# Kernel optimization log

Measured on AMD Instinct MI355X. Metric: run time of the kernel, lower is better.

## Reference

```python
import jax, jax.numpy as jnp
import numpy as np
from jax import lax

B, C, H, W = 2, 128, 192, 192
HEADS, WS, SS = 4, 8, 4
HID = 256  # int(C * expansion=2.0)
EPS = 1e-6


def _rpe_index(ws):
    coords = np.stack(np.meshgrid(np.arange(ws), np.arange(ws), indexing='ij')).reshape(2, -1)
    rel = (coords[:, :, None] - coords[:, None, :]).transpose(1, 2, 0)
    rel[:, :, 0] += ws - 1
    rel[:, :, 1] += ws - 1
    rel[:, :, 0] *= 2 * ws - 1
    return rel.sum(-1)  # (ws^2, ws^2) int index into rpe_table

RPE_IDX = _rpe_index(WS)


def _attn_mask(hp, wp, ws, ss):
    # Swin-style shifted-window mask, built once for static (hp, wp).
    img = np.zeros((hp, wp))
    cnt = 0
    for hs in (slice(0, -ws), slice(-ws, -ss), slice(-ss, None)):
        for wsl in (slice(0, -ws), slice(-ws, -ss), slice(-ss, None)):
            img[hs, wsl] = cnt
            cnt += 1
    mw = img.reshape(hp // ws, ws, wp // ws, ws).transpose(0, 2, 1, 3).reshape(-1, ws * ws)
    am = mw[:, None, :] - mw[:, :, None]
    return np.where(am != 0, -np.inf, 0.0).astype(np.float32)

MASK = jnp.asarray(_attn_mask(H, W, WS, SS))  # (nW, T, T)


def rmsnorm(x, s, b):
    # RMSNorm2d: variance over channel dim, computed in fp32.
    var = jnp.mean(jnp.square(x.astype(jnp.float32)), axis=1, keepdims=True)
    rms = jnp.sqrt(var + EPS).astype(x.dtype)
    return s[None, :, None, None] * x / rms + b[None, :, None, None]


def conv1x1(x, w, b):
    return jnp.einsum('oc,bchw->bohw', w, x) + b[None, :, None, None]


def dwconv3x3(x, w, b):
    y = lax.conv_general_dilated(x, w, (1, 1), 'SAME', feature_group_count=w.shape[0],
                                 dimension_numbers=('NCHW', 'OIHW', 'NCHW'))
    return y + b[None, :, None, None]


def gelu(x):
    return jax.nn.gelu(x, approximate=False)  # matches torch nn.GELU default (erf)


def conv_gated_block(x, s, b, w1, b1, wd, bd, w2, b2, beta):
    y = rmsnorm(x, s, b)
    y = conv1x1(y, w1, b1)
    y = dwconv3x3(y, wd, bd)
    u, v = jnp.split(y, 2, axis=1)
    y = conv1x1(u * gelu(v), w2, b2)
    return x + beta * y


def gated_ffn(x, s, b, w1, b1, w2, b2, gamma):
    y = rmsnorm(x, s, b)
    y = conv1x1(y, w1, b1)
    u, v = jnp.split(y, 2, axis=1)
    y = conv1x1(u * gelu(v), w2, b2)
    return x + gamma * y


def window_attention(x, qkv_w, qkv_b, rpe_table, proj_w, proj_b):
    b, c, h, w = x.shape
    hd = c // HEADS
    ws, ws2 = WS, WS * WS
    # H, W chosen divisible by ws, so _pad_to_window is a no-op here.
    x = jnp.roll(x, (-SS, -SS), axis=(2, 3))
    qkv = jnp.einsum('oc,bchw->bhwo', qkv_w, x) + qkv_b  # (B,H,W,3C)
    qkv = qkv.reshape(b, h // ws, ws, w // ws, ws, 3 * c).transpose(0, 1, 3, 2, 4, 5)
    qkv = qkv.reshape(-1, ws2, 3, HEADS, hd).transpose(2, 0, 3, 1, 4)  # (3, B*nW, nh, T, hd)
    q, k, v = qkv[0], qkv[1], qkv[2]
    attn = jnp.einsum('wnqd,wnkd->wnqk', q, k) * (hd ** -0.5)
    rpe = rpe_table[RPE_IDX.reshape(-1)].reshape(ws2, ws2, HEADS).transpose(2, 0, 1)  # (nh,T,T)
    nW = (h // ws) * (w // ws)
    attn = attn.reshape(b, nW, HEADS, ws2, ws2) + rpe[None, None] + MASK[None, :, None]
    attn = jax.nn.softmax(attn, axis=-1).reshape(-1, HEADS, ws2, ws2)
    out = jnp.einsum('wnqk,wnkd->wnqd', attn, v)
    out = out.transpose(0, 2, 1, 3).reshape(-1, ws2, c)
    out = out @ proj_w.T + proj_b  # nn.Linear
    out = out.reshape(b, h // ws, w // ws, ws, ws, c).transpose(0, 1, 3, 2, 4, 5).reshape(b, h, w, c)
    out = jnp.roll(out, (SS, SS), axis=(1, 2))
    return out.transpose(0, 3, 1, 2)


def setup_inputs():
    key = jax.random.key(0)
    ks = jax.random.split(key, 10)
    f = jnp.float32

    def nrm(k, shape, std=0.02):
        return jax.random.normal(k, shape, dtype=f) * std

    return {
        'x': jax.random.normal(ks[0], (B, C, H, W), dtype=f),
        'cg_s': jnp.ones((C,), f), 'cg_b': jnp.zeros((C,), f),
        'pw1_w': nrm(ks[1], (2 * HID, C)), 'pw1_b': jnp.zeros((2 * HID,), f),
        'dw_w': nrm(ks[2], (2 * HID, 1, 3, 3)), 'dw_b': jnp.zeros((2 * HID,), f),
        'pw2_w': nrm(ks[3], (C, HID)), 'pw2_b': jnp.zeros((C,), f),
        'beta': jnp.float32(0.5),
        'at_s': jnp.ones((C,), f), 'at_b': jnp.zeros((C,), f),
        'qkv_w': nrm(ks[4], (3 * C, C)), 'qkv_b': jnp.zeros((3 * C,), f),
        'rpe_table': nrm(ks[5], ((2 * WS - 1) ** 2, HEADS)),
        'proj_w': nrm(ks[6], (C, C)), 'proj_b': jnp.zeros((C,), f),
        'alpha': jnp.float32(0.5),
        'ff_s': jnp.ones((C,), f), 'ff_b': jnp.zeros((C,), f),
        'fc1_w': nrm(ks[7], (2 * HID, C)), 'fc1_b': jnp.zeros((2 * HID,), f),
        'fc2_w': nrm(ks[8], (C, HID)), 'fc2_b': jnp.zeros((C,), f),
        'gamma': jnp.float32(0.5),
    }


def reference(x, cg_s, cg_b, pw1_w, pw1_b, dw_w, dw_b, pw2_w, pw2_b, beta,
              at_s, at_b, qkv_w, qkv_b, rpe_table, proj_w, proj_b, alpha,
              ff_s, ff_b, fc1_w, fc1_b, fc2_w, fc2_b, gamma):
    x = conv_gated_block(x, cg_s, cg_b, pw1_w, pw1_b, dw_w, dw_b, pw2_w, pw2_b, beta)
    x = x + alpha * window_attention(rmsnorm(x, at_s, at_b), qkv_w, qkv_b, rpe_table, proj_w, proj_b)
    x = gated_ffn(x, ff_s, ff_b, fc1_w, fc1_b, fc2_w, fc2_b, gamma)
    return x
```

## Files before the change

### kernel.cpp

```cpp
#include <hip/hip_runtime.h>
#include <hip/hip_bf16.h>
#include <math.h>

#define HW   36864
#define BHW  73728

typedef float f32x4 __attribute__((ext_vector_type(4)));
typedef short short8 __attribute__((ext_vector_type(8)));

__device__ __forceinline__ unsigned f2bf(float f) {
    unsigned u = __float_as_uint(f);
    return (u + 0x7fffu + ((u >> 16) & 1u)) >> 16;
}
__device__ __forceinline__ float bf2f(unsigned short s) {
    return __uint_as_float(((unsigned)s) << 16);
}
__device__ __forceinline__ float gelu_erf(float v) {
    return v * 0.5f * (1.0f + erff(v * 0.70710678118654752f));
}

__global__ __launch_bounds__(256)
void wconv_kernel(const float* __restrict__ w1, const float* __restrict__ w2,
                  const float* __restrict__ wq, const float* __restrict__ wp,
                  const float* __restrict__ wf1, const float* __restrict__ wf2,
                  const float* __restrict__ dww, const float* __restrict__ fb1,
                  ushort* __restrict__ o1, ushort* __restrict__ o2, ushort* __restrict__ oq,
                  ushort* __restrict__ op, ushort* __restrict__ of1, ushort* __restrict__ of2,
                  float* __restrict__ dwt, float* __restrict__ bg)
{
    int i = blockIdx.x * 256 + threadIdx.x;
    if      (i <  65536) o1 [i         ] = (ushort)f2bf(w1 [i         ]);
    else if (i <  98304) o2 [i -  65536] = (ushort)f2bf(w2 [i -  65536]);
    else if (i < 147456) oq [i -  98304] = (ushort)f2bf(wq [i -  98304]);
    else if (i < 163840) op [i - 147456] = (ushort)f2bf(wp [i - 147456]);
    else if (i < 229376) {
        int j = i - 163840;
        int col = j >> 7, k = j & 127;
        of1[j] = (ushort)f2bf(wf1[((size_t)((col & 1) * 256 + (col >> 1))) * 128 + k]);
    }
    else if (i < 262144) of2[i - 229376] = (ushort)f2bf(wf2[i - 229376]);
    else if (i < 266752) {
        int j = i - 262144;
        int tap = j >> 9, c = j & 511;
        dwt[j] = dww[c * 9 + tap];
    }
    else if (i < 267264) {
        int j = i - 266752;
        bg[j] = fb1[(j & 1) * 256 + (j >> 1)];
    }
}

__global__ __launch_bounds__(256)
void rmsnorm_t_kernel(const float* __restrict__ src, const float* __restrict__ s,
                      const float* __restrict__ bi, __hip_bfloat16* __restrict__ dst)
{
    int P = blockIdx.x * 256 + threadIdx.x;
    int b = P / HW, pp = P - b * HW;
    const float* xb = src + (size_t)b * 128 * HW + pp;
    float ss = 0.f;
#pragma unroll 8
    for (int c = 0; c < 128; ++c) { float v = xb[(size_t)c * HW]; ss = fmaf(v, v, ss); }
    float inv = 1.0f / sqrtf(ss * 0.0078125f + 1e-6f);
    unsigned* drow = (unsigned*)(dst + (size_t)P * 128);
#pragma unroll 4
    for (int c = 0; c < 128; c += 2) {
        float v0 = fmaf(s[c]     * xb[(size_t)c * HW],       inv, bi[c]);
        float v1 = fmaf(s[c + 1] * xb[(size_t)(c + 1) * HW], inv, bi[c + 1]);
        drow[c >> 1] = f2bf(v0) | (f2bf(v1) << 16);
    }
}

template<int K, int MODE>
__global__ __launch_bounds__(256)
void gemm_kernel(const __hip_bfloat16* __restrict__ Abf, const __hip_bfloat16* __restrict__ Wbf,
                 const float* __restrict__ bias, int N,
                 __hip_bfloat16* __restrict__ outb,
                 const float* __restrict__ rsrc, float* __restrict__ rdst,
                 const float* __restrict__ scale,
                 const float* __restrict__ rms_s, const float* __restrict__ rms_b,
                 __hip_bfloat16* __restrict__ xn)
{
    constexpr int SMEM = (MODE == 3) ? 56320 : ((MODE == 1) ? 34816 : 16384);
    __shared__ char smem[SMEM];
    short* sA = (short*)smem;
    short* sB = sA + 4096;
    float* sEp = (float*)smem;
    float* sPar = (float*)(smem + 34816);
    float* sInv = (float*)(smem + 39168);
    ushort* sXn = (ushort*)(smem + 39424);

    const short* A = (const short*)Abf;
    const short* W = (const short*)Wbf;

    int t = threadIdx.x;
    int lane = t & 63, wv = t >> 6;
    int wm = wv & 1, wn = wv >> 1;
    int m0 = blockIdx.x * 128;
    int n0 = blockIdx.y * 128;
    int q = lane >> 4, r16 = lane & 15;

    f32x4 acc[4][4];
#pragma unroll
    for (int nt = 0; nt < 4; ++nt) {
        float bv = bias[n0 + wn * 64 + nt * 16 + r16];
#pragma unroll
        for (int mt = 0; mt < 4; ++mt) acc[mt][nt] = (f32x4){bv, bv, bv, bv};
    }

    for (int kk = 0; kk < K; kk += 32) {
#pragma unroll
        for (int i = 0; i < 2; ++i) {
            int rbase = wv * 32 + i * 16;
            int row = rbase + (lane >> 2);
            int kc = (lane & 3) ^ ((row >> 1) & 3);
            const short* ga = A + (size_t)(m0 + row) * K + kk + kc * 8;
            const short* gb = W + (size_t)(n0 + row) * K + kk + kc * 8;
            __builtin_amdgcn_global_load_lds((const __attribute__((address_space(1))) void*)ga,
                                             (__attribute__((address_space(3))) void*)(sA + rbase * 32), 16, 0, 0);
            __builtin_amdgcn_global_load_lds((const __attribute__((address_space(1))) void*)gb,
                                             (__attribute__((address_space(3))) void*)(sB + rbase * 32), 16, 0, 0);
        }
        __syncthreads();

        short8 af[4], bf[4];
#pragma unroll
        for (int mt = 0; mt < 4; ++mt) {
            int r = wm * 64 + mt * 16 + r16;
            af[mt] = *(const short8*)(sA + (r * 4 + (q ^ ((r >> 1) & 3))) * 8);
        }
#pragma unroll
        for (int nt = 0; nt < 4; ++nt) {
            int r = wn * 64 + nt * 16 + r16;
            bf[nt] = *(const short8*)(sB + (r * 4 + (q ^ ((r >> 1) & 3))) * 8);
        }
#pragma unroll
        for (int mt = 0; mt < 4; ++mt)
#pragma unroll
            for (int nt = 0; nt < 4; ++nt)
                acc[mt][nt] = __builtin_amdgcn_mfma_f32_16x16x32_bf16(af[mt], bf[nt], acc[mt][nt], 0, 0, 0);
        __syncthreads();
    }

    if constexpr (MODE == 0) {
        ushort* ob = (ushort*)outb;
#pragma unroll
        for (int mt = 0; mt < 4; ++mt) {
            int row0 = m0 + wm * 64 + mt * 16 + q * 4;
#pragma unroll
            for (int nt = 0; nt < 4; ++nt) {
                int col = n0 + wn * 64 + nt * 16 + r16;
#pragma unroll
                for (int rg = 0; rg < 4; ++rg)
                    ob[(size_t)(row0 + rg) * N + col] = (ushort)f2bf(acc[mt][nt][rg]);
            }
        }
    } else if constexpr (MODE == 2) {
        ushort* ob = (ushort*)outb;
        int parity = r16 & 1;
#pragma unroll
        for (int mt = 0; mt < 4; ++mt) {
            int row0 = m0 + wm * 64 + mt * 16 + q * 4;
#pragma unroll
            for (int nt = 0; nt < 4; ++nt) {
                int ch = (n0 + wn * 64 + nt * 16 + r16) >> 1;
#pragma unroll
                for (int rg = 0; rg < 4; ++rg) {
                    float val = acc[mt][nt][rg];
                    float part = __shfl_xor(val, 1);
                    float uu = parity ? part : val;
                    float vv = parity ? val : part;
                    float g = uu * gelu_erf(vv);
                    if (!parity)
                        ob[(size_t)(row0 + rg) * 256 + ch] = (ushort)f2bf(g);
                }
            }
        }
    } else {
        float sc = scale[0];
        for (int h = 0; h < 2; ++h) {
            __syncthreads();
            if (wm == h) {
#pragma unroll
                for (int mt = 0; mt < 4; ++mt)
#pragma unroll
                    for (int nt = 0; nt < 4; ++nt) {
                        int c = wn * 64 + nt * 16 + r16;
                        int px = mt * 16 + q * 4;
#pragma unroll
                        for (int rg = 0; rg < 4; ++rg)
                            sEp[c * 68 + px + rg] = acc[mt][nt][rg];
                    }
            }
            __syncthreads();
            int c16 = t >> 4, l16 = t & 15;
            int p0 = m0 + h * 64 + l16 * 4;
            int b = p0 / HW, pp = p0 - b * HW;
            f32x4 ov[8];
            f32x4 ps = (f32x4){0.f, 0.f, 0.f, 0.f};
#pragma unroll
            for (int i = 0; i < 8; ++i) {
                int c = c16 + i * 16;
                f32x4 v = *(const f32x4*)&sEp[c * 68 + l16 * 4];
                size_t gi = (size_t)(b * 128 + c) * HW + pp;
                f32x4 r = *(const f32x4*)&rsrc[gi];
                f32x4 o = r + sc * v;
                *(f32x4*)&rdst[gi] = o;
                if constexpr (MODE == 3) {
                    ov[i] = o;
#pragma unroll
                    for (int rg = 0; rg < 4; ++rg) ps[rg] = fmaf(o[rg], o[rg], ps[rg]);
                }
            }
            if constexpr (MODE == 3) {
#pragma unroll
                for (int rg = 0; rg < 4; ++rg) sPar[(l16 * 4 + rg) * 17 + c16] = ps[rg];
                __syncthreads();
                if (t < 64) {
                    float ssum = 0.f;
#pragma unroll
                    for (int j = 0; j < 16; ++j) ssum += sPar[t * 17 + j];
                    sInv[t] = 1.0f / sqrtf(ssum * 0.0078125f + 1e-6f);
                }
                __syncthreads();
                float iv[4];
#pragma unroll
                for (int rg = 0; rg < 4; ++rg) iv[rg] = sInv[l16 * 4 + rg];
#pragma unroll
                for (int i = 0; i < 8; ++i) {
                    int c = c16 + i * 16;
                    float scs = rms_s[c], bcs = rms_b[c];
#pragma unroll
                    for (int rg = 0; rg < 4; ++rg)
                        sXn[(l16 * 4 + rg) * 132 + c] = (ushort)f2bf(fmaf(scs * ov[i][rg], iv[rg], bcs));
                }
                __syncthreads();
                {
                    int px = t >> 2, qd = t & 3;
                    const ushort* src = sXn + px * 132 + qd * 32;
                    ushort* dst = (ushort*)xn + (size_t)(m0 + h * 64 + px) * 128 + qd * 32;
#pragma unroll
                    for (int g = 0; g < 4; ++g)
                        *(short8*)(dst + g * 8) = *(const short8*)(src + g * 8);
                }
            }
        }
    }
}

__global__ __launch_bounds__(256)
void dwgate_kernel(const __hip_bfloat16* __restrict__ t1, const float* __restrict__ dwt,
                   const float* __restrict__ dwb, __hip_bfloat16* __restrict__ tg)
{
    int t = threadIdx.x;
    int c8 = t & 31, pxl = t >> 5;
    int bx = blockIdx.x;
    int wseg = bx % 24; int tmp = bx / 24;
    int hp2 = tmp % 96; int b = tmp / 96;
    int h0 = hp2 * 2, w = wseg * 8 + pxl;
    int cu = c8 * 8;
    const ushort* t1u = (const ushort*)t1;

    float au[2][8], av[2][8];
    {
        f32x4 b0 = *(const f32x4*)(dwb + cu);
        f32x4 b1 = *(const f32x4*)(dwb + cu + 4);
        f32x4 b2 = *(const f32x4*)(dwb + 256 + cu);
        f32x4 b3 = *(const f32x4*)(dwb + 256 + cu + 4);
#pragma unroll
        for (int e = 0; e < 4; ++e) {
            au[0][e] = au[1][e] = b0[e]; au[0][e + 4] = au[1][e + 4] = b1[e];
            av[0][e] = av[1][e] = b2[e]; av[0][e + 4] = av[1][e + 4] = b3[e];
        }
    }
#pragma unroll
    for (int r = 0; r < 4; ++r) {
        int hh = h0 - 1 + r;
        if (hh < 0 || hh >= 192) continue;
#pragma unroll
        for (int dxi = 0; dxi < 3; ++dxi) {
            int w2 = w + dxi - 1;
            if (w2 < 0 || w2 >= 192) continue;
            const ushort* urow = t1u + (size_t)(b * HW + hh * 192 + w2) * 512 + cu;
            short8 u8 = *(const short8*)urow;
            short8 v8 = *(const short8*)(urow + 256);
#pragma unroll
            for (int py = 0; py < 2; ++py) {
                int dy = r - 1 - py;
                if (dy < -1 || dy > 1) continue;
                int tap = (dy + 1) * 3 + dxi;
                f32x4 wu0 = *(const f32x4*)(dwt + tap * 512 + cu);
                f32x4 wu1 = *(const f32x4*)(dwt + tap * 512 + cu + 4);
                f32x4 wv0 = *(const f32x4*)(dwt + tap * 512 + 256 + cu);
                f32x4 wv1 = *(const f32x4*)(dwt + tap * 512 + 256 + cu + 4);
#pragma unroll
                for (int e = 0; e < 4; ++e) {
                    au[py][e]     = fmaf(wu0[e], bf2f((ushort)u8[e]),     au[py][e]);
                    au[py][e + 4] = fmaf(wu1[e], bf2f((ushort)u8[e + 4]), au[py][e + 4]);
                    av[py][e]     = fmaf(wv0[e], bf2f((ushort)v8[e]),     av[py][e]);
                    av[py][e + 4] = fmaf(wv1[e], bf2f((ushort)v8[e + 4]), av[py][e + 4]);
                }
            }
        }
    }
#pragma unroll
    for (int py = 0; py < 2; ++py) {
        short8 o8;
#pragma unroll
        for (int e = 0; e < 8; ++e) o8[e] = (short)(ushort)f2bf(au[py][e] * gelu_erf(av[py][e]));
        int gp = b * HW + (h0 + py) * 192 + w;
        *(short8*)((ushort*)tg + (size_t)gp * 256 + cu) = o8;
    }
}

__device__ __forceinline__ int wpix(int wh, int ww, int m) {
    int ty = m >> 3, tx = m & 7;
    int hs = wh * 8 + ty + 4; if (hs >= 192) hs -= 192;
    int wsc = ww * 8 + tx + 4; if (wsc >= 192) wsc -= 192;
    return hs * 192 + wsc;
}
__device__ __forceinline__ int wreg(int wh, int ww, int m) {
    int hr = wh * 8 + (m >> 3), wr = ww * 8 + (m & 7);
    return ((hr < 184) ? 0 : (hr < 188) ? 1 : 2) * 3 +
           ((wr < 184) ? 0 : (wr < 188) ? 1 : 2);
}

__global__ __launch_bounds__(256)
void attn_kernel(const __hip_bfloat16* __restrict__ qkv, const float* __restrict__ rpe,
                 __hip_bfloat16* __restrict__ attnout)
{
    __shared__ char smem[54288];
    int t = threadIdx.x;
    int lane = t & 63, head = t >> 6;
    int wh = blockIdx.x / 24, ww = blockIdx.x % 24;
    int b = blockIdx.y;
    int q = lane >> 4, r16 = lane & 15;

    float* rpe_s = (float*)(smem + 50688);
    for (int i = t; i < 900; i += 256) rpe_s[i] = rpe[i];

    char* Pbuf  = smem + head * 12672;
    char* VTbuf = Pbuf + 8448;
    const ushort* qkvu = (const ushort*)qkv;

    short8 aq[4], bk[4];
#pragma unroll
    for (int mt = 0; mt < 4; ++mt) {
        int pix = wpix(wh, ww, mt * 16 + r16);
        const ushort* rowp = qkvu + (size_t)(b * HW + pix) * 384 + head * 32 + q * 8;
        aq[mt] = *(const short8*)rowp;
        bk[mt] = *(const short8*)(rowp + 128);
    }
    {
        int pix = wpix(wh, ww, lane);
        const ushort* vp = qkvu + (size_t)(b * HW + pix) * 384 + 256 + head * 32;
        ushort* vt = (ushort*)VTbuf;
#pragma unroll
        for (int g = 0; g < 4; ++g) {
            short8 v8 = *(const short8*)(vp + g * 8);
#pragma unroll
            for (int e = 0; e < 8; ++e) vt[(g * 8 + e) * 66 + lane] = (ushort)v8[e];
        }
    }
    __syncthreads();

    f32x4 s[4][4];
#pragma unroll
    for (int mt = 0; mt < 4; ++mt)
#pragma unroll
        for (int nt = 0; nt < 4; ++nt) s[mt][nt] = (f32x4){0.f, 0.f, 0.f, 0.f};
#pragma unroll
    for (int mt = 0; mt < 4; ++mt)
#pragma unroll
        for (int nt = 0; nt < 4; ++nt)
            s[mt][nt] = __builtin_amdgcn_mfma_f32_16x16x32_bf16(aq[mt], bk[nt], s[mt][nt], 0, 0, 0);

    bool edge = (wh == 23) || (ww == 23);
    int tyj[4], txj[4], rgj[4];
#pragma unroll
    for (int nt = 0; nt < 4; ++nt) {
        int j = nt * 16 + r16;
        tyj[nt] = j >> 3; txj[nt] = j & 7;
        rgj[nt] = wreg(wh, ww, j);
    }
    float rinv[4][4];
#pragma unroll
    for (int mt = 0; mt < 4; ++mt) {
#pragma unroll
        for (int rg = 0; rg < 4; ++rg) {
            int i = mt * 16 + q * 4 + rg;
            int tyi = i >> 3, txi = i & 7;
            int rgi = edge ? wreg(wh, ww, i) : 0;
            float mx = -INFINITY;
#pragma unroll
            for (int nt = 0; nt < 4; ++nt) {
                float v = s[mt][nt][rg] * 0.17677669529663689f
                        + rpe_s[((tyi - tyj[nt] + 7) * 15 + (txi - txj[nt] + 7)) * 4 + head];
                if (edge && rgi != rgj[nt]) v = -INFINITY;
                s[mt][nt][rg] = v;
                mx = fmaxf(mx, v);
            }
            mx = fmaxf(mx, __shfl_xor(mx, 1));
            mx = fmaxf(mx, __shfl_xor(mx, 2));
            mx = fmaxf(mx, __shfl_xor(mx, 4));
            mx = fmaxf(mx, __shfl_xor(mx, 8));
            float sum = 0.f;
#pragma unroll
            for (int nt = 0; nt < 4; ++nt) {
                float e = __expf(s[mt][nt][rg] - mx);
                s[mt][nt][rg] = e;
                sum += e;
            }
            sum += __shfl_xor(sum, 1);
            sum += __shfl_xor(sum, 2);
            sum += __shfl_xor(sum, 4);
            sum += __shfl_xor(sum, 8);
            rinv[mt][rg] = 1.0f / sum;
        }
    }

    ushort* Pu = (ushort*)Pbuf;
#pragma unroll
    for (int mt = 0; mt < 4; ++mt)
#pragma unroll
        for (int rg = 0; rg < 4; ++rg) {
            int i = mt * 16 + q * 4 + rg;
#pragma unroll
            for (int nt = 0; nt < 4; ++nt)
                Pu[i * 66 + nt * 16 + r16] = (ushort)f2bf(s[mt][nt][rg]);
        }
    __syncthreads();

    f32x4 o[4][2];
#pragma unroll
    for (int mt = 0; mt < 4; ++mt) { o[mt][0] = (f32x4){0,0,0,0}; o[mt][1] = (f32x4){0,0,0,0}; }
    const uint* Pw = (const uint*)Pbuf;
    const uint* Vw = (const uint*)VTbuf;
#pragma unroll
    for (int ks = 0; ks < 2; ++ks) {
        short8 ap[4];
#pragma unroll
        for (int mt = 0; mt < 4; ++mt) {
            int base = (mt * 16 + r16) * 33 + ks * 16 + q * 4;
            uint d0 = Pw[base], d1 = Pw[base + 1], d2 = Pw[base + 2], d3 = Pw[base + 3];
            union { uint u[4]; short8 s8; } cv; cv.u[0] = d0; cv.u[1] = d1; cv.u[2] = d2; cv.u[3] = d3;
            ap[mt] = cv.s8;
        }
        short8 bv[2];
#pragma unroll
        for (int nt = 0; nt < 2; ++nt) {
            int base = (nt * 16 + r16) * 33 + ks * 16 + q * 4;
            uint d0 = Vw[base], d1 = Vw[base + 1], d2 = Vw[base + 2], d3 = Vw[base + 3];
            union { uint u[4]; short8 s8; } cv; cv.u[0] = d0; cv.u[1] = d1; cv.u[2] = d2; cv.u[3] = d3;
            bv[nt] = cv.s8;
        }
#pragma unroll
        for (int mt = 0; mt < 4; ++mt)
#pragma unroll
            for (int nt = 0; nt < 2; ++nt)
                o[mt][nt] = __builtin_amdgcn_mfma_f32_16x16x32_bf16(ap[mt], bv[nt], o[mt][nt], 0, 0, 0);
    }
    __syncthreads();

    float* Of = (float*)Pbuf;
#pragma unroll
    for (int mt = 0; mt < 4; ++mt)
#pragma unroll
        for (int rg = 0; rg < 4; ++rg) {
            int i = mt * 16 + q * 4 + rg;
            float sc = rinv[mt][rg];
            Of[i * 33 + r16]      = o[mt][0][rg] * sc;
            Of[i * 33 + 16 + r16] = o[mt][1][rg] * sc;
        }
    __syncthreads();
    {
        int pix = wpix(wh, ww, lane);
        ushort* ob = (ushort*)attnout + (size_t)(b * HW + pix) * 128 + head * 32;
#pragma unroll
        for (int g = 0; g < 4; ++g) {
            short8 o8;
#pragma unroll
            for (int e = 0; e < 8; ++e) o8[e] = (short)(ushort)f2bf(Of[lane * 33 + g * 8 + e]);
            *(short8*)(ob + g * 8) = o8;
        }
    }
}

extern "C" void kernel_launch(void* const* d_in, const int* in_sizes, int n_in,
                              void* d_out, int out_size, void* d_ws, size_t ws_size,
                              hipStream_t stream)
{
    const float* x     = (const float*)d_in[0];
    const float* cg_s  = (const float*)d_in[1];
    const float* cg_b  = (const float*)d_in[2];
    const float* pw1_w = (const float*)d_in[3];
    const float* pw1_b = (const float*)d_in[4];
    const float* dw_w  = (const float*)d_in[5];
    const float* dw_b  = (const float*)d_in[6];
    const float* pw2_w = (const float*)d_in[7];
    const float* pw2_b = (const float*)d_in[8];
    const float* beta  = (const float*)d_in[9];
    const float* at_s  = (const float*)d_in[10];
    const float* at_b  = (const float*)d_in[11];
    const float* qkv_w = (const float*)d_in[12];
    const float* qkv_b = (const float*)d_in[13];
    const float* rpe   = (const float*)d_in[14];
    const float* proj_w= (const float*)d_in[15];
    const float* proj_b= (const float*)d_in[16];
    const float* alpha = (const float*)d_in[17];
    const float* ff_s  = (const float*)d_in[18];
    const float* ff_b  = (const float*)d_in[19];
    const float* fc1_w = (const float*)d_in[20];
    const float* fc1_b = (const float*)d_in[21];
    const float* fc2_w = (const float*)d_in[22];
    const float* fc2_b = (const float*)d_in[23];
    const float* gamma = (const float*)d_in[24];
    float* out = (float*)d_out;

    char* ws = (char*)d_ws;
    __hip_bfloat16* Xn    = (__hip_bfloat16*)ws;
    __hip_bfloat16* t1    = (__hip_bfloat16*)(ws + 18874368);
    __hip_bfloat16* qkvb  = t1;
    __hip_bfloat16* tg    = (__hip_bfloat16*)(ws + 94371840);
    __hip_bfloat16* attno = tg;
    char* wsw = ws + 132120576;
    ushort* w1b  = (ushort*)(wsw);
    ushort* w2b  = (ushort*)(wsw + 131072);
    ushort* wqb  = (ushort*)(wsw + 196608);
    ushort* wpb  = (ushort*)(wsw + 294912);
    ushort* wf1b = (ushort*)(wsw + 327680);
    ushort* wf2b = (ushort*)(wsw + 458752);
    float*  dwt  = (float*) (wsw + 524288);
    float*  bg1  = (float*) (wsw + 542720);

    wconv_kernel<<<1044, 256, 0, stream>>>(pw1_w, pw2_w, qkv_w, proj_w, fc1_w, fc2_w, dw_w, fc1_b,
                                           w1b, w2b, wqb, wpb, wf1b, wf2b, dwt, bg1);

    rmsnorm_t_kernel<<<288, 256, 0, stream>>>(x, cg_s, cg_b, Xn);
    gemm_kernel<128, 0><<<dim3(576, 4), 256, 0, stream>>>(Xn, (__hip_bfloat16*)w1b, pw1_b, 512, t1,
                                                          nullptr, nullptr, nullptr, nullptr, nullptr, nullptr);
    dwgate_kernel<<<4608, 256, 0, stream>>>(t1, dwt, dw_b, tg);
    gemm_kernel<256, 3><<<dim3(576, 1), 256, 0, stream>>>(tg, (__hip_bfloat16*)w2b, pw2_b, 128, nullptr,
                                                          x, out, beta, at_s, at_b, Xn);

    gemm_kernel<128, 0><<<dim3(576, 3), 256, 0, stream>>>(Xn, (__hip_bfloat16*)wqb, qkv_b, 384, qkvb,
                                                          nullptr, nullptr, nullptr, nullptr, nullptr, nullptr);
    attn_kernel<<<dim3(576, 2), 256, 0, stream>>>(qkvb, rpe, attno);
    gemm_kernel<128, 3><<<dim3(576, 1), 256, 0, stream>>>(attno, (__hip_bfloat16*)wpb, proj_b, 128, nullptr,
                                                          out, out, alpha, ff_s, ff_b, Xn);

    gemm_kernel<128, 2><<<dim3(576, 4), 256, 0, stream>>>(Xn, (__hip_bfloat16*)wf1b, bg1, 512, tg,
                                                          nullptr, nullptr, nullptr, nullptr, nullptr, nullptr);
    gemm_kernel<256, 1><<<dim3(576, 1), 256, 0, stream>>>(tg, (__hip_bfloat16*)wf2b, fc2_b, 128, nullptr,
                                                          out, out, gamma, nullptr, nullptr, nullptr);
}
```

Baseline: 410.5 us.

## Stage GEMM epilogue stores through LDS and retile depthwise gate kernel

The MODE 0 and MODE 2 GEMM epilogues now write bf16 results into a padded shared-memory tile and then emit coalesced 16-byte row stores, replacing scattered 2-byte global writes. The depthwise-conv gate kernel is retiled so each thread handles 4 channels over 4 output rows. It preloads all 9 tap weights into registers and uses branchless clamped loads, which cuts reloads of weights and overlapping input rows. This adds extra syncs and LDS traffic in the GEMMs and raises register pressure in the dwconv kernel, with launch bounds set for 3 blocks per SIMD.

```diff
diff --git a/kernel.cpp b/kernel.cpp
--- a/kernel.cpp
+++ b/kernel.cpp
@@ -7,6 +7,7 @@
 
 typedef float f32x4 __attribute__((ext_vector_type(4)));
 typedef short short8 __attribute__((ext_vector_type(8)));
+typedef short s16x4 __attribute__((ext_vector_type(4)));
 
 __device__ __forceinline__ unsigned f2bf(float f) {
     unsigned u = __float_as_uint(f);
@@ -80,7 +81,8 @@
                  const float* __restrict__ rms_s, const float* __restrict__ rms_b,
                  __hip_bfloat16* __restrict__ xn)
 {
-    constexpr int SMEM = (MODE == 3) ? 56320 : ((MODE == 1) ? 34816 : 16384);
+    constexpr int SMEM = (MODE == 3) ? 56320 : ((MODE == 1) ? 34816 :
+                         ((MODE == 0) ? 17408 : 16384));
     __shared__ char smem[SMEM];
     short* sA = (short*)smem;
     short* sB = sA + 4096;
@@ -142,37 +144,62 @@
     }
 
     if constexpr (MODE == 0) {
+        ushort* sC = (ushort*)smem;
         ushort* ob = (ushort*)outb;
-#pragma unroll
-        for (int mt = 0; mt < 4; ++mt) {
-            int row0 = m0 + wm * 64 + mt * 16 + q * 4;
-#pragma unroll
-            for (int nt = 0; nt < 4; ++nt) {
-                int col = n0 + wn * 64 + nt * 16 + r16;
-#pragma unroll
-                for (int rg = 0; rg < 4; ++rg)
-                    ob[(size_t)(row0 + rg) * N + col] = (ushort)f2bf(acc[mt][nt][rg]);
+        for (int h = 0; h < 2; ++h) {
+            __syncthreads();
+            if (wm == h) {
+#pragma unroll
+                for (int mt = 0; mt < 4; ++mt)
+#pragma unroll
+                    for (int nt = 0; nt < 4; ++nt) {
+                        int row = mt * 16 + q * 4;
+                        int col = wn * 64 + nt * 16 + r16;
+#pragma unroll
+                        for (int rg = 0; rg < 4; ++rg)
+                            sC[(row + rg) * 136 + col] = (ushort)f2bf(acc[mt][nt][rg]);
+                    }
+            }
+            __syncthreads();
+            int px = t >> 2, ck = t & 3;
+            size_t base = (size_t)(m0 + h * 64 + px) * N + n0;
+#pragma unroll
+            for (int g = 0; g < 4; ++g) {
+                int co = (ck * 4 + g) * 8;
+                *(short8*)(ob + base + co) = *(const short8*)(sC + px * 136 + co);
             }
         }
     } else if constexpr (MODE == 2) {
+        ushort* sG = (ushort*)smem;
         ushort* ob = (ushort*)outb;
         int parity = r16 & 1;
-#pragma unroll
-        for (int mt = 0; mt < 4; ++mt) {
-            int row0 = m0 + wm * 64 + mt * 16 + q * 4;
-#pragma unroll
-            for (int nt = 0; nt < 4; ++nt) {
-                int ch = (n0 + wn * 64 + nt * 16 + r16) >> 1;
-#pragma unroll
-                for (int rg = 0; rg < 4; ++rg) {
-                    float val = acc[mt][nt][rg];
-                    float part = __shfl_xor(val, 1);
-                    float uu = parity ? part : val;
-                    float vv = parity ? val : part;
-                    float g = uu * gelu_erf(vv);
-                    if (!parity)
-                        ob[(size_t)(row0 + rg) * 256 + ch] = (ushort)f2bf(g);
-                }
+        for (int h = 0; h < 2; ++h) {
+            __syncthreads();
+            if (wm == h) {
+#pragma unroll
+                for (int mt = 0; mt < 4; ++mt)
+#pragma unroll
+                    for (int nt = 0; nt < 4; ++nt) {
+                        int row = mt * 16 + q * 4;
+                        int gch = (wn * 64 + nt * 16 + r16) >> 1;
+#pragma unroll
+                        for (int rg = 0; rg < 4; ++rg) {
+                            float val = acc[mt][nt][rg];
+                            float part = __shfl_xor(val, 1);
+                            float uu = parity ? part : val;
+                            float vv = parity ? val : part;
+                            float g = uu * gelu_erf(vv);
+                            if (!parity) sG[(row + rg) * 72 + gch] = (ushort)f2bf(g);
+                        }
+                    }
+            }
+            __syncthreads();
+            int px = t >> 2, ck = t & 3;
+            size_t base = (size_t)(m0 + h * 64 + px) * 256 + (n0 >> 1);
+#pragma unroll
+            for (int g = 0; g < 2; ++g) {
+                int co = (ck * 2 + g) * 8;
+                *(short8*)(ob + base + co) = *(const short8*)(sG + px * 72 + co);
             }
         }
     } else {
@@ -247,68 +274,73 @@
     }
 }
 
-__global__ __launch_bounds__(256)
+__global__ __launch_bounds__(256, 3)
 void dwgate_kernel(const __hip_bfloat16* __restrict__ t1, const float* __restrict__ dwt,
                    const float* __restrict__ dwb, __hip_bfloat16* __restrict__ tg)
 {
     int t = threadIdx.x;
-    int c8 = t & 31, pxl = t >> 5;
+    int tc = t & 15;
+    int tp = t >> 4;
     int bx = blockIdx.x;
-    int wseg = bx % 24; int tmp = bx / 24;
-    int hp2 = tmp % 96; int b = tmp / 96;
-    int h0 = hp2 * 2, w = wseg * 8 + pxl;
-    int cu = c8 * 8;
+    int wseg = bx % 12; int tmp = bx / 12;
+    int hq = tmp % 48; int b = tmp / 48;
+    int cu = blockIdx.y * 64 + tc * 4;
+    int h0 = hq * 4;
+    int w = wseg * 16 + tp;
     const ushort* t1u = (const ushort*)t1;
 
-    float au[2][8], av[2][8];
-    {
-        f32x4 b0 = *(const f32x4*)(dwb + cu);
-        f32x4 b1 = *(const f32x4*)(dwb + cu + 4);
-        f32x4 b2 = *(const f32x4*)(dwb + 256 + cu);
-        f32x4 b3 = *(const f32x4*)(dwb + 256 + cu + 4);
-#pragma unroll
-        for (int e = 0; e < 4; ++e) {
-            au[0][e] = au[1][e] = b0[e]; au[0][e + 4] = au[1][e + 4] = b1[e];
-            av[0][e] = av[1][e] = b2[e]; av[0][e + 4] = av[1][e + 4] = b3[e];
-        }
-    }
-#pragma unroll
-    for (int r = 0; r < 4; ++r) {
+    f32x4 wu[9], wv[9];
+#pragma unroll
+    for (int tap = 0; tap < 9; ++tap) {
+        wu[tap] = *(const f32x4*)(dwt + tap * 512 + cu);
+        wv[tap] = *(const f32x4*)(dwt + tap * 512 + 256 + cu);
+    }
+    f32x4 bu = *(const f32x4*)(dwb + cu);
+    f32x4 bv = *(const f32x4*)(dwb + 256 + cu);
+
+    f32x4 au[4], av[4];
+#pragma unroll
+    for (int py = 0; py < 4; ++py) { au[py] = bu; av[py] = bv; }
+
+#pragma unroll
+    for (int r = 0; r < 6; ++r) {
         int hh = h0 - 1 + r;
-        if (hh < 0 || hh >= 192) continue;
+        bool okr = (unsigned)hh < 192u;
+        int hhc = okr ? hh : 0;
 #pragma unroll
         for (int dxi = 0; dxi < 3; ++dxi) {
             int w2 = w + dxi - 1;
-            if (w2 < 0 || w2 >= 192) continue;
-            const ushort* urow = t1u + (size_t)(b * HW + hh * 192 + w2) * 512 + cu;
-            short8 u8 = *(const short8*)urow;
-            short8 v8 = *(const short8*)(urow + 256);
-#pragma unroll
-            for (int py = 0; py < 2; ++py) {
+            bool ok = okr && ((unsigned)w2 < 192u);
+            int w2c = (w2 < 0) ? 0 : ((w2 > 191) ? 191 : w2);
+            const ushort* p = t1u + (size_t)(b * HW + hhc * 192 + w2c) * 512 + cu;
+            s16x4 u4 = *(const s16x4*)p;
+            s16x4 v4 = *(const s16x4*)(p + 256);
+            f32x4 uf, vf;
+#pragma unroll
+            for (int e = 0; e < 4; ++e) {
+                uf[e] = ok ? bf2f((ushort)u4[e]) : 0.f;
+                vf[e] = ok ? bf2f((ushort)v4[e]) : 0.f;
+            }
+#pragma unroll
+            for (int py = 0; py < 4; ++py) {
                 int dy = r - 1 - py;
                 if (dy < -1 || dy > 1) continue;
                 int tap = (dy + 1) * 3 + dxi;
-                f32x4 wu0 = *(const f32x4*)(dwt + tap * 512 + cu);
-                f32x4 wu1 = *(const f32x4*)(dwt + tap * 512 + cu + 4);
-                f32x4 wv0 = *(const f32x4*)(dwt + tap * 512 + 256 + cu);
-                f32x4 wv1 = *(const f32x4*)(dwt + tap * 512 + 256 + cu + 4);
 #pragma unroll
                 for (int e = 0; e < 4; ++e) {
-                    au[py][e]     = fmaf(wu0[e], bf2f((ushort)u8[e]),     au[py][e]);
-                    au[py][e + 4] = fmaf(wu1[e], bf2f((ushort)u8[e + 4]), au[py][e + 4]);
-                    av[py][e]     = fmaf(wv0[e], bf2f((ushort)v8[e]),     av[py][e]);
-                    av[py][e + 4] = fmaf(wv1[e], bf2f((ushort)v8[e + 4]), av[py][e + 4]);
+                    au[py][e] = fmaf(wu[tap][e], uf[e], au[py][e]);
+                    av[py][e] = fmaf(wv[tap][e], vf[e], av[py][e]);
                 }
             }
         }
     }
 #pragma unroll
-    for (int py = 0; py < 2; ++py) {
-        short8 o8;
-#pragma unroll
-        for (int e = 0; e < 8; ++e) o8[e] = (short)(ushort)f2bf(au[py][e] * gelu_erf(av[py][e]));
+    for (int py = 0; py < 4; ++py) {
+        s16x4 o4;
+#pragma unroll
+        for (int e = 0; e < 4; ++e) o4[e] = (short)(ushort)f2bf(au[py][e] * gelu_erf(av[py][e]));
         int gp = b * HW + (h0 + py) * 192 + w;
-        *(short8*)((ushort*)tg + (size_t)gp * 256 + cu) = o8;
+        *(s16x4*)((ushort*)tg + (size_t)gp * 256 + cu) = o4;
     }
 }
 
@@ -538,7 +570,7 @@
     rmsnorm_t_kernel<<<288, 256, 0, stream>>>(x, cg_s, cg_b, Xn);
     gemm_kernel<128, 0><<<dim3(576, 4), 256, 0, stream>>>(Xn, (__hip_bfloat16*)w1b, pw1_b, 512, t1,
                                                           nullptr, nullptr, nullptr, nullptr, nullptr, nullptr);
-    dwgate_kernel<<<4608, 256, 0, stream>>>(t1, dwt, dw_b, tg);
+    dwgate_kernel<<<dim3(1152, 4), 256, 0, stream>>>(t1, dwt, dw_b, tg);
     gemm_kernel<256, 3><<<dim3(576, 1), 256, 0, stream>>>(tg, (__hip_bfloat16*)w2b, pw2_b, 128, nullptr,
                                                           x, out, beta, at_s, at_b, Xn);
 
```

Result: slower. 462.8 us (+12.8%).
